# Kernel tuning notes

Measured on AMD Instinct MI355X. Metric: run time of the kernel, lower is better.

## Reference

```python
import jax, jax.numpy as jnp
import numpy as np

BIGNET_DIM = 1024
N_LAYERS = 18   # 6 blocks * 3 QLoRALinear
N_LN = 5
GROUPS = 64     # 1024 / group_size(16)
GS = 16
RANK = 32
BATCH = 16384
EPS = 1e-5


def dequant(qw, scale):
    # qw: [O, G, gs] int 0..15, scale: [O, G] per-group max-abs norm
    w = (qw.astype(jnp.float32) / 15.0 * 2.0 - 1.0) * scale[..., None]
    return w.reshape(qw.shape[0], -1)  # [O, I]


def qlora_linear(x, qw, scale, b, a_w, b_w):
    w = dequant(qw, scale)                      # [O, I]
    base = x @ w.T + b                          # [N, O]
    lora = (x @ a_w.T) @ b_w.T                  # [N, r] @ [r, O]
    return base + lora


def layernorm(h, g, b):
    mu = h.mean(-1, keepdims=True)
    var = jnp.mean((h - mu) ** 2, -1, keepdims=True)
    return (h - mu) * jax.lax.rsqrt(var + EPS) * g + b


def setup_inputs() -> dict:
    key = jax.random.key(0)
    ks = jax.random.split(key, 8)
    x = jax.random.normal(ks[0], (BATCH, BIGNET_DIM), jnp.float32)
    qw = jax.random.randint(ks[1], (N_LAYERS, BIGNET_DIM, GROUPS, GS), 0, 16, jnp.int32)
    scale = jax.random.uniform(ks[2], (N_LAYERS, BIGNET_DIM, GROUPS), jnp.float32) * 0.05
    bias = jax.random.normal(ks[3], (N_LAYERS, BIGNET_DIM), jnp.float32) * 0.02
    la = jax.random.normal(ks[4], (N_LAYERS, RANK, BIGNET_DIM), jnp.float32) * (2.0 / BIGNET_DIM) ** 0.5
    # note: torch zero-inits lora_b; use small random values so the LoRA path is testable
    lb = jax.random.normal(ks[5], (N_LAYERS, BIGNET_DIM, RANK), jnp.float32) * 0.01
    ln_w = jnp.ones((N_LN, BIGNET_DIM), jnp.float32)
    ln_b = jnp.zeros((N_LN, BIGNET_DIM), jnp.float32)
    return {"x": x, "scale": scale, "bias": bias, "la": la, "lb": lb,
            "ln_w": ln_w, "ln_b": ln_b, "qw": qw}


def reference(x, scale, bias, la, lb, ln_w, ln_b, qw):
    h = x
    li = 0
    for blk in range(6):
        r = h
        for j in range(3):
            h = qlora_linear(h, qw[li], scale[li], bias[li], la[li], lb[li])
            li += 1
            if j < 2:
                h = jax.nn.relu(h)
        h = h + r
        if blk < 5:
            h = layernorm(h, ln_w[blk], ln_b[blk])
    return h
```

## Files before the change

kernel.cpp:

```cpp
#include <hip/hip_runtime.h>

typedef unsigned short UST;
typedef __attribute__((ext_vector_type(8))) __bf16 bf16x8;
typedef __attribute__((ext_vector_type(4))) float f32x4;

__device__ __forceinline__ float bf2f(UST u) {
    union { unsigned int i; float f; } v; v.i = ((unsigned int)u) << 16; return v.f;
}
__device__ __forceinline__ UST f2bf(float f) {
    union { float f; unsigned int i; } v; v.f = f;
    return (UST)((v.i + 0x7fffu + ((v.i >> 16) & 1u)) >> 16);
}

__device__ __forceinline__ void gl2lds16(const UST* g, UST* l) {
    __builtin_amdgcn_global_load_lds(
        (const __attribute__((address_space(1))) unsigned int*)g,
        (__attribute__((address_space(3))) unsigned int*)l, 16, 0, 0);
}

__global__ __launch_bounds__(256) void prep_w(
    const int* __restrict__ qw, const float* __restrict__ scale,
    const float* __restrict__ la, const float* __restrict__ lb,
    UST* __restrict__ wp)
{
    int l = blockIdx.x, ot = blockIdx.y, it = blockIdx.z;
    __shared__ float la_s[32 * 128];
    __shared__ float lb_s[64 * 33];
    int t = threadIdx.x;
    int o0 = (t >> 4) * 4;
    int i0 = (t & 15) * 8;

    const int* qbase = qw + (size_t)l * 1048576 + (size_t)(ot * 64 + o0) * 1024
                       + it * 128 + i0;
    int4 qv[8];
    #pragma unroll
    for (int a = 0; a < 4; a++) {
        qv[2 * a]     = *(const int4*)(qbase + (size_t)a * 1024);
        qv[2 * a + 1] = *(const int4*)(qbase + (size_t)a * 1024 + 4);
    }
    const float* sL = scale + (size_t)l * 65536;
    float sc[4];
    #pragma unroll
    for (int a = 0; a < 4; a++)
        sc[a] = sL[(size_t)(ot * 64 + o0 + a) * 64 + ((it * 128 + i0) >> 4)];

    const float* laL = la + (size_t)l * 32768;
    const float* lbL = lb + (size_t)l * 32768 + (size_t)ot * 64 * 32;
    for (int e = t; e < 32 * 128; e += 256) {
        int r = e >> 7, i = e & 127;
        la_s[e] = laL[r * 1024 + it * 128 + i];
    }
    for (int e = t; e < 64 * 32; e += 256) {
        int o = e >> 5, r = e & 31;
        lb_s[o * 33 + r] = lbL[e];
    }
    __syncthreads();

    float acc[4][8];
    #pragma unroll
    for (int a = 0; a < 4; a++)
        #pragma unroll
        for (int c = 0; c < 8; c++) acc[a][c] = 0.f;
    for (int r = 0; r < 32; ++r) {
        float4 av0 = *(const float4*)&la_s[r * 128 + i0];
        float4 av1 = *(const float4*)&la_s[r * 128 + i0 + 4];
        float av[8] = {av0.x, av0.y, av0.z, av0.w, av1.x, av1.y, av1.z, av1.w};
        float bv[4];
        #pragma unroll
        for (int j = 0; j < 4; j++) bv[j] = lb_s[(o0 + j) * 33 + r];
        #pragma unroll
        for (int a = 0; a < 4; a++)
            #pragma unroll
            for (int c = 0; c < 8; c++) acc[a][c] += bv[a] * av[c];
    }

    UST* wL = wp + (size_t)l * 1048576;
    #pragma unroll
    for (int a = 0; a < 4; a++) {
        int go = ot * 64 + o0 + a;
        int gi = it * 128 + i0;
        float s = sc[a];
        int q[8];
        q[0] = qv[2 * a].x; q[1] = qv[2 * a].y; q[2] = qv[2 * a].z; q[3] = qv[2 * a].w;
        q[4] = qv[2 * a + 1].x; q[5] = qv[2 * a + 1].y;
        q[6] = qv[2 * a + 1].z; q[7] = qv[2 * a + 1].w;
        UST o8[8];
        #pragma unroll
        for (int c = 0; c < 8; c++) {
            float w = ((float)q[c] * (2.0f / 15.0f) - 1.0f) * s + acc[a][c];
            o8[c] = f2bf(w);
        }
        *(ushort4*)(wL + (size_t)go * 1024 + gi) = make_ushort4(o8[0], o8[1], o8[2], o8[3]);
        *(ushort4*)(wL + (size_t)go * 1024 + gi + 4) = make_ushort4(o8[4], o8[5], o8[6], o8[7]);
    }
}

__global__ __launch_bounds__(256) void f32_to_bf16(const float* __restrict__ x,
                                                   UST* __restrict__ o)
{
    size_t i = ((size_t)blockIdx.x * 256 + threadIdx.x) * 4;
    float4 v = *(const float4*)(x + i);
    *(ushort4*)(o + i) = make_ushort4(f2bf(v.x), f2bf(v.y), f2bf(v.z), f2bf(v.w));
}

#define BM 128
#define BN 128
#define BK 32

#define WB4 asm volatile("s_waitcnt vmcnt(4)\n\ts_barrier" ::: "memory")
#define WB0 asm volatile("s_waitcnt vmcnt(0)\n\ts_barrier" ::: "memory")
#define LGB asm volatile("s_waitcnt lgkmcnt(0)\n\ts_barrier" ::: "memory")

__global__ __launch_bounds__(256, 4) void gemm_ep(
    const UST* __restrict__ X, const UST* __restrict__ W,
    const float* __restrict__ bias,
    UST* __restrict__ outb, const UST* __restrict__ resid,
    float* __restrict__ outf, int mode)
{
    const int K = 1024;
    __shared__ UST smem[16384];
    int tid = threadIdx.x;
    int wave = tid >> 6, lane = tid & 63;
    int wm = wave >> 1, wn = wave & 1;

    int bid = blockIdx.x;
    int nbm8 = gridDim.x >> 6;
    int xcd = bid & 7, idx = bid >> 3;
    int bm = xcd + ((idx % nbm8) << 3);
    int bn = idx / nbm8;

    int la15 = lane & 15, qa = lane >> 4;

    int c0 = tid, c1 = tid + 256;
    int r0 = c0 >> 2, k0c = ((c0 & 3) ^ ((r0 >> 1) & 3)) * 8;
    int r1 = c1 >> 2, k1c = ((c1 & 3) ^ ((r1 >> 1) & 3)) * 8;
    const UST* gA0 = X + (size_t)(bm * BM + r0) * K + k0c;
    const UST* gA1 = X + (size_t)(bm * BM + r1) * K + k1c;
    const UST* gB0 = W + (size_t)(bn * BN + r0) * K + k0c;
    const UST* gB1 = W + (size_t)(bn * BN + r1) * K + k1c;

    int offA[4], offB[4];
    #pragma unroll
    for (int i = 0; i < 4; i++) {
        int ra = wm * 64 + i * 16 + la15;
        offA[i] = ra * 32 + ((qa ^ ((ra >> 1) & 3)) * 8);
        int rb = wn * 64 + i * 16 + la15;
        offB[i] = rb * 32 + ((qa ^ ((rb >> 1) & 3)) * 8);
    }

    f32x4 acc[4][4];
    #pragma unroll
    for (int i = 0; i < 4; i++)
        #pragma unroll
        for (int j = 0; j < 4; j++) acc[i][j] = (f32x4){0.f, 0.f, 0.f, 0.f};

    auto issue = [&](int kk, int buf) {
        UST* dA = smem + buf * 8192;
        UST* dB = dA + 4096;
        gl2lds16(gA0 + kk, dA + c0 * 8);
        gl2lds16(gA1 + kk, dA + c1 * 8);
        gl2lds16(gB0 + kk, dB + c0 * 8);
        gl2lds16(gB1 + kk, dB + c1 * 8);
    };
    auto compute = [&](int buf) {
        const UST* pA = smem + buf * 8192;
        const UST* pB = pA + 4096;
        bf16x8 af[4], bfr[4];
        #pragma unroll
        for (int mi = 0; mi < 4; mi++) af[mi] = *(const bf16x8*)&pA[offA[mi]];
        #pragma unroll
        for (int ni = 0; ni < 4; ni++) bfr[ni] = *(const bf16x8*)&pB[offB[ni]];
        #pragma unroll
        for (int mi = 0; mi < 4; mi++)
            #pragma unroll
            for (int ni = 0; ni < 4; ni++)
                acc[mi][ni] = __builtin_amdgcn_mfma_f32_16x16x32_bf16(
                    af[mi], bfr[ni], acc[mi][ni], 0, 0, 0);
    };

    issue(0, 0);
    #pragma unroll 2
    for (int it = 0; it < 31; ++it) {
        int cur = it & 1;
        issue((it + 1) * BK, cur ^ 1);
        WB4;
        compute(cur);
        LGB;
    }
    WB0;
    compute(1);
    LGB;

    float* cs = (float*)smem;
    int cc = tid & 15, rw = tid >> 4;
    int gcolb = bn * BN + cc * 8;
    float4 bv0 = *(const float4*)&bias[gcolb];
    float4 bv1 = *(const float4*)&bias[gcolb + 4];

    #pragma unroll
    for (int h = 0; h < 2; ++h) {
        if (wm == h) {
            #pragma unroll
            for (int mi = 0; mi < 4; mi++)
                #pragma unroll
                for (int ni = 0; ni < 4; ni++) {
                    int colx = (wn * 64 + ni * 16 + la15) ^ (qa << 4);
                    #pragma unroll
                    for (int r2 = 0; r2 < 4; r2++) {
                        int rl = mi * 16 + qa * 4 + r2;
                        cs[rl * 128 + colx] = acc[mi][ni][r2];
                    }
                }
        }
        LGB;
        #pragma unroll
        for (int g = 0; g < 4; ++g) {
            int rl = g * 16 + rw;
            int swz = ((rl >> 2) & 3) << 2;
            int gr0 = ((cc * 2) ^ swz) * 4;
            float4 v0 = *(const float4*)&cs[rl * 128 + gr0];
            float4 v1 = *(const float4*)&cs[rl * 128 + gr0 + 4];
            float o0 = v0.x + bv0.x, o1 = v0.y + bv0.y;
            float o2 = v0.z + bv0.z, o3 = v0.w + bv0.w;
            float o4 = v1.x + bv1.x, o5 = v1.y + bv1.y;
            float o6 = v1.z + bv1.z, o7 = v1.w + bv1.w;
            if (mode == 0) {
                o0 = fmaxf(o0, 0.f); o1 = fmaxf(o1, 0.f);
                o2 = fmaxf(o2, 0.f); o3 = fmaxf(o3, 0.f);
                o4 = fmaxf(o4, 0.f); o5 = fmaxf(o5, 0.f);
                o6 = fmaxf(o6, 0.f); o7 = fmaxf(o7, 0.f);
            }
            int grow = bm * BM + h * 64 + rl;
            size_t base = (size_t)grow * 1024 + gcolb;
            if (mode == 2) {
                ushort4 rv0 = *(const ushort4*)&resid[base];
                ushort4 rv1 = *(const ushort4*)&resid[base + 4];
                o0 += bf2f(rv0.x); o1 += bf2f(rv0.y);
                o2 += bf2f(rv0.z); o3 += bf2f(rv0.w);
                o4 += bf2f(rv1.x); o5 += bf2f(rv1.y);
                o6 += bf2f(rv1.z); o7 += bf2f(rv1.w);
                *(float4*)&outf[base] = make_float4(o0, o1, o2, o3);
                *(float4*)&outf[base + 4] = make_float4(o4, o5, o6, o7);
            } else {
                uint4 pk;
                pk.x = (unsigned)f2bf(o0) | ((unsigned)f2bf(o1) << 16);
                pk.y = (unsigned)f2bf(o2) | ((unsigned)f2bf(o3) << 16);
                pk.z = (unsigned)f2bf(o4) | ((unsigned)f2bf(o5) << 16);
                pk.w = (unsigned)f2bf(o6) | ((unsigned)f2bf(o7) << 16);
                *(uint4*)&outb[base] = pk;
            }
        }
        LGB;
    }
}

__global__ __launch_bounds__(256) void ln_res(
    const UST* __restrict__ h3, UST* __restrict__ r,
    const float* __restrict__ g, const float* __restrict__ b)
{
    int row = blockIdx.x;
    int t = threadIdx.x;
    int lane = t & 63, wave = t >> 6;
    const ushort4* hp = (const ushort4*)(h3 + (size_t)row * 1024);
    ushort4* rp = (ushort4*)(r + (size_t)row * 1024);
    ushort4 hv = hp[t], rv = rp[t];
    float u0 = bf2f(hv.x) + bf2f(rv.x);
    float u1 = bf2f(hv.y) + bf2f(rv.y);
    float u2 = bf2f(hv.z) + bf2f(rv.z);
    float u3 = bf2f(hv.w) + bf2f(rv.w);

    float s = u0 + u1 + u2 + u3;
    #pragma unroll
    for (int off = 32; off > 0; off >>= 1) s += __shfl_down(s, off, 64);
    __shared__ float red[8];
    if (lane == 0) red[wave] = s;
    __syncthreads();
    float mean = (red[0] + red[1] + red[2] + red[3]) * (1.0f / 1024.0f);

    float d0 = u0 - mean, d1 = u1 - mean, d2 = u2 - mean, d3 = u3 - mean;
    float vs = d0 * d0 + d1 * d1 + d2 * d2 + d3 * d3;
    #pragma unroll
    for (int off = 32; off > 0; off >>= 1) vs += __shfl_down(vs, off, 64);
    if (lane == 0) red[4 + wave] = vs;
    __syncthreads();
    float var = (red[4] + red[5] + red[6] + red[7]) * (1.0f / 1024.0f);
    float rstd = rsqrtf(var + 1e-5f);

    int i0 = t * 4;
    ushort4 o;
    o.x = f2bf(d0 * rstd * g[i0 + 0] + b[i0 + 0]);
    o.y = f2bf(d1 * rstd * g[i0 + 1] + b[i0 + 1]);
    o.z = f2bf(d2 * rstd * g[i0 + 2] + b[i0 + 2]);
    o.w = f2bf(d3 * rstd * g[i0 + 3] + b[i0 + 3]);
    rp[t] = o;
}

extern "C" void kernel_launch(void* const* d_in, const int* in_sizes, int n_in,
                              void* d_out, int out_size, void* d_ws, size_t ws_size,
                              hipStream_t stream) {
    const float* x     = (const float*)d_in[0];
    const float* scale = (const float*)d_in[1];
    const float* bias  = (const float*)d_in[2];
    const float* la    = (const float*)d_in[3];
    const float* lb    = (const float*)d_in[4];
    const float* ln_w  = (const float*)d_in[5];
    const float* ln_b  = (const float*)d_in[6];
    const int*   qw    = (const int*)d_in[7];

    const int M = in_sizes[0] / 1024;
    const size_t WPB = (size_t)18 * 1024 * 1024 * 2;
    const size_t ACT = (size_t)M * 1024 * 2;

    UST* wp = (UST*)d_ws;
    UST* A  = (UST*)((char*)d_ws + WPB);
    UST* Cb = (UST*)((char*)d_ws + WPB + ACT);
    UST* Bb = (UST*)d_out;

    prep_w<<<dim3(18, 16, 8), 256, 0, stream>>>(qw, scale, la, lb, wp);
    f32_to_bf16<<<(M * 1024) / (256 * 4), 256, 0, stream>>>(x, A);

    int nblk = (M / 128) * 8;
    int li = 0;
    for (int blk = 0; blk < 6; ++blk) {
        gemm_ep<<<nblk, 256, 0, stream>>>(
            A, wp + (size_t)li * 1024 * 1024, bias + li * 1024, Bb, nullptr, nullptr, 0);
        li++;
        gemm_ep<<<nblk, 256, 0, stream>>>(
            Bb, wp + (size_t)li * 1024 * 1024, bias + li * 1024, Cb, nullptr, nullptr, 0);
        li++;
        if (blk < 5) {
            gemm_ep<<<nblk, 256, 0, stream>>>(
                Cb, wp + (size_t)li * 1024 * 1024, bias + li * 1024, Bb, nullptr, nullptr, 1);
            li++;
            ln_res<<<M, 256, 0, stream>>>(Bb, A, ln_w + blk * 1024, ln_b + blk * 1024);
        } else {
            gemm_ep<<<nblk, 256, 0, stream>>>(
                Cb, wp + (size_t)li * 1024 * 1024, bias + li * 1024, nullptr, A,
                (float*)d_out, 2);
            li++;
        }
    }
}
```

Measured before the change: 1.097 ms.

## Enlarge GEMM tiles to 256x256 with 512 threads and MFMA-based weight prep

The main GEMM now uses a 256x256 output tile with 8 waves (512 threads), each wave computing 64x128. The goal is more reuse per LDS load and half as many global loads of A and W per output element. The weight-prep kernel now computes the LoRA product lb·la with bf16 MFMA instead of scalar FMAs and fuses dequantisation into an LDS-staged transposed store. The costs are higher register pressure (32 accumulators per wave), 64KB of LDS per block, and fewer blocks in the grid, which may lower occupancy. The LoRA product is also rounded to bf16 inputs before the matmul.

```diff
diff --git a/kernel.cpp b/kernel.cpp
--- a/kernel.cpp
+++ b/kernel.cpp
@@ -17,6 +17,10 @@
         (const __attribute__((address_space(1))) unsigned int*)g,
         (__attribute__((address_space(3))) unsigned int*)l, 16, 0, 0);
 }
+
+#define WB4 asm volatile("s_waitcnt vmcnt(4)\n\ts_barrier" ::: "memory")
+#define WB0 asm volatile("s_waitcnt vmcnt(0)\n\ts_barrier" ::: "memory")
+#define LGB asm volatile("s_waitcnt lgkmcnt(0)\n\ts_barrier" ::: "memory")
 
 __global__ __launch_bounds__(256) void prep_w(
     const int* __restrict__ qw, const float* __restrict__ scale,
@@ -24,179 +28,68 @@
     UST* __restrict__ wp)
 {
     int l = blockIdx.x, ot = blockIdx.y, it = blockIdx.z;
-    __shared__ float la_s[32 * 128];
-    __shared__ float lb_s[64 * 33];
+    __shared__ float cs[64 * 128];
+    __shared__ float sc_s[128 * 8];
     int t = threadIdx.x;
-    int o0 = (t >> 4) * 4;
-    int i0 = (t & 15) * 8;
-
-    const int* qbase = qw + (size_t)l * 1048576 + (size_t)(ot * 64 + o0) * 1024
-                       + it * 128 + i0;
-    int4 qv[8];
-    #pragma unroll
-    for (int a = 0; a < 4; a++) {
-        qv[2 * a]     = *(const int4*)(qbase + (size_t)a * 1024);
-        qv[2 * a + 1] = *(const int4*)(qbase + (size_t)a * 1024 + 4);
-    }
-    const float* sL = scale + (size_t)l * 65536;
-    float sc[4];
-    #pragma unroll
-    for (int a = 0; a < 4; a++)
-        sc[a] = sL[(size_t)(ot * 64 + o0 + a) * 64 + ((it * 128 + i0) >> 4)];
-
-    const float* laL = la + (size_t)l * 32768;
-    const float* lbL = lb + (size_t)l * 32768 + (size_t)ot * 64 * 32;
-    for (int e = t; e < 32 * 128; e += 256) {
-        int r = e >> 7, i = e & 127;
-        la_s[e] = laL[r * 1024 + it * 128 + i];
-    }
-    for (int e = t; e < 64 * 32; e += 256) {
-        int o = e >> 5, r = e & 31;
-        lb_s[o * 33 + r] = lbL[e];
-    }
+    int wave = t >> 6, lane = t & 63;
+    int wm = wave >> 1, wn = wave & 1;
+    int la15 = lane & 15, qa = lane >> 4;
+
+    {
+        int e = t * 4;
+        int o = e >> 3, g = e & 7;
+        const float* sb = scale + ((size_t)l * 1024 + ot * 128 + o) * 64 + it * 8 + g;
+        *(float4*)&sc_s[e] = *(const float4*)sb;
+    }
+
+    bf16x8 af[4];
+    const float* lbL = lb + ((size_t)l * 1024 + ot * 128 + wm * 64 + la15) * 32 + qa * 8;
+    #pragma unroll
+    for (int mi = 0; mi < 4; mi++) {
+        float4 u0 = *(const float4*)(lbL + mi * 16 * 32);
+        float4 u1 = *(const float4*)(lbL + mi * 16 * 32 + 4);
+        union { bf16x8 v; UST u[8]; } A;
+        A.u[0] = f2bf(u0.x); A.u[1] = f2bf(u0.y); A.u[2] = f2bf(u0.z); A.u[3] = f2bf(u0.w);
+        A.u[4] = f2bf(u1.x); A.u[5] = f2bf(u1.y); A.u[6] = f2bf(u1.z); A.u[7] = f2bf(u1.w);
+        af[mi] = A.v;
+    }
+
+    bf16x8 bfr[4];
+    const float* laL = la + ((size_t)l * 32 + qa * 8) * 1024 + it * 128 + wn * 64 + la15;
+    #pragma unroll
+    for (int ni = 0; ni < 4; ni++) {
+        union { bf16x8 v; UST u[8]; } B;
+        #pragma unroll
+        for (int j = 0; j < 8; j++) B.u[j] = f2bf(laL[(size_t)j * 1024 + ni * 16]);
+        bfr[ni] = B.v;
+    }
+
+    f32x4 acc[4][4];
+    #pragma unroll
+    for (int mi = 0; mi < 4; mi++)
+        #pragma unroll
+        for (int ni = 0; ni < 4; ni++) {
+            acc[mi][ni] = (f32x4){0.f, 0.f, 0.f, 0.f};
+            acc[mi][ni] = __builtin_amdgcn_mfma_f32_16x16x32_bf16(
+                af[mi], bfr[ni], acc[mi][ni], 0, 0, 0);
+        }
+
+    int qv[4][4][4];
+    const int* qL = qw + (size_t)l * 1048576;
+    int obase = ot * 128 + wm * 64, ibase = it * 128 + wn * 64;
+    #pragma unroll
+    for (int mi = 0; mi < 4; mi++)
+        #pragma unroll
+        for (int ni = 0; ni < 4; ni++)
+            #pragma unroll
+            for (int r2 = 0; r2 < 4; r2++)
+                qv[mi][ni][r2] = qL[(size_t)(obase + mi * 16 + qa * 4 + r2) * 1024
+                                    + ibase + ni * 16 + la15];
+
     __syncthreads();
 
-    float acc[4][8];
-    #pragma unroll
-    for (int a = 0; a < 4; a++)
-        #pragma unroll
-        for (int c = 0; c < 8; c++) acc[a][c] = 0.f;
-    for (int r = 0; r < 32; ++r) {
-        float4 av0 = *(const float4*)&la_s[r * 128 + i0];
-        float4 av1 = *(const float4*)&la_s[r * 128 + i0 + 4];
-        float av[8] = {av0.x, av0.y, av0.z, av0.w, av1.x, av1.y, av1.z, av1.w};
-        float bv[4];
-        #pragma unroll
-        for (int j = 0; j < 4; j++) bv[j] = lb_s[(o0 + j) * 33 + r];
-        #pragma unroll
-        for (int a = 0; a < 4; a++)
-            #pragma unroll
-            for (int c = 0; c < 8; c++) acc[a][c] += bv[a] * av[c];
-    }
-
+    int cc = t & 15, rw = t >> 4;
     UST* wL = wp + (size_t)l * 1048576;
-    #pragma unroll
-    for (int a = 0; a < 4; a++) {
-        int go = ot * 64 + o0 + a;
-        int gi = it * 128 + i0;
-        float s = sc[a];
-        int q[8];
-        q[0] = qv[2 * a].x; q[1] = qv[2 * a].y; q[2] = qv[2 * a].z; q[3] = qv[2 * a].w;
-        q[4] = qv[2 * a + 1].x; q[5] = qv[2 * a + 1].y;
-        q[6] = qv[2 * a + 1].z; q[7] = qv[2 * a + 1].w;
-        UST o8[8];
-        #pragma unroll
-        for (int c = 0; c < 8; c++) {
-            float w = ((float)q[c] * (2.0f / 15.0f) - 1.0f) * s + acc[a][c];
-            o8[c] = f2bf(w);
-        }
-        *(ushort4*)(wL + (size_t)go * 1024 + gi) = make_ushort4(o8[0], o8[1], o8[2], o8[3]);
-        *(ushort4*)(wL + (size_t)go * 1024 + gi + 4) = make_ushort4(o8[4], o8[5], o8[6], o8[7]);
-    }
-}
-
-__global__ __launch_bounds__(256) void f32_to_bf16(const float* __restrict__ x,
-                                                   UST* __restrict__ o)
-{
-    size_t i = ((size_t)blockIdx.x * 256 + threadIdx.x) * 4;
-    float4 v = *(const float4*)(x + i);
-    *(ushort4*)(o + i) = make_ushort4(f2bf(v.x), f2bf(v.y), f2bf(v.z), f2bf(v.w));
-}
-
-#define BM 128
-#define BN 128
-#define BK 32
-
-#define WB4 asm volatile("s_waitcnt vmcnt(4)\n\ts_barrier" ::: "memory")
-#define WB0 asm volatile("s_waitcnt vmcnt(0)\n\ts_barrier" ::: "memory")
-#define LGB asm volatile("s_waitcnt lgkmcnt(0)\n\ts_barrier" ::: "memory")
-
-__global__ __launch_bounds__(256, 4) void gemm_ep(
-    const UST* __restrict__ X, const UST* __restrict__ W,
-    const float* __restrict__ bias,
-    UST* __restrict__ outb, const UST* __restrict__ resid,
-    float* __restrict__ outf, int mode)
-{
-    const int K = 1024;
-    __shared__ UST smem[16384];
-    int tid = threadIdx.x;
-    int wave = tid >> 6, lane = tid & 63;
-    int wm = wave >> 1, wn = wave & 1;
-
-    int bid = blockIdx.x;
-    int nbm8 = gridDim.x >> 6;
-    int xcd = bid & 7, idx = bid >> 3;
-    int bm = xcd + ((idx % nbm8) << 3);
-    int bn = idx / nbm8;
-
-    int la15 = lane & 15, qa = lane >> 4;
-
-    int c0 = tid, c1 = tid + 256;
-    int r0 = c0 >> 2, k0c = ((c0 & 3) ^ ((r0 >> 1) & 3)) * 8;
-    int r1 = c1 >> 2, k1c = ((c1 & 3) ^ ((r1 >> 1) & 3)) * 8;
-    const UST* gA0 = X + (size_t)(bm * BM + r0) * K + k0c;
-    const UST* gA1 = X + (size_t)(bm * BM + r1) * K + k1c;
-    const UST* gB0 = W + (size_t)(bn * BN + r0) * K + k0c;
-    const UST* gB1 = W + (size_t)(bn * BN + r1) * K + k1c;
-
-    int offA[4], offB[4];
-    #pragma unroll
-    for (int i = 0; i < 4; i++) {
-        int ra = wm * 64 + i * 16 + la15;
-        offA[i] = ra * 32 + ((qa ^ ((ra >> 1) & 3)) * 8);
-        int rb = wn * 64 + i * 16 + la15;
-        offB[i] = rb * 32 + ((qa ^ ((rb >> 1) & 3)) * 8);
-    }
-
-    f32x4 acc[4][4];
-    #pragma unroll
-    for (int i = 0; i < 4; i++)
-        #pragma unroll
-        for (int j = 0; j < 4; j++) acc[i][j] = (f32x4){0.f, 0.f, 0.f, 0.f};
-
-    auto issue = [&](int kk, int buf) {
-        UST* dA = smem + buf * 8192;
-        UST* dB = dA + 4096;
-        gl2lds16(gA0 + kk, dA + c0 * 8);
-        gl2lds16(gA1 + kk, dA + c1 * 8);
-        gl2lds16(gB0 + kk, dB + c0 * 8);
-        gl2lds16(gB1 + kk, dB + c1 * 8);
-    };
-    auto compute = [&](int buf) {
-        const UST* pA = smem + buf * 8192;
-        const UST* pB = pA + 4096;
-        bf16x8 af[4], bfr[4];
-        #pragma unroll
-        for (int mi = 0; mi < 4; mi++) af[mi] = *(const bf16x8*)&pA[offA[mi]];
-        #pragma unroll
-        for (int ni = 0; ni < 4; ni++) bfr[ni] = *(const bf16x8*)&pB[offB[ni]];
-        #pragma unroll
-        for (int mi = 0; mi < 4; mi++)
-            #pragma unroll
-            for (int ni = 0; ni < 4; ni++)
-                acc[mi][ni] = __builtin_amdgcn_mfma_f32_16x16x32_bf16(
-                    af[mi], bfr[ni], acc[mi][ni], 0, 0, 0);
-    };
-
-    issue(0, 0);
-    #pragma unroll 2
-    for (int it = 0; it < 31; ++it) {
-        int cur = it & 1;
-        issue((it + 1) * BK, cur ^ 1);
-        WB4;
-        compute(cur);
-        LGB;
-    }
-    WB0;
-    compute(1);
-    LGB;
-
-    float* cs = (float*)smem;
-    int cc = tid & 15, rw = tid >> 4;
-    int gcolb = bn * BN + cc * 8;
-    float4 bv0 = *(const float4*)&bias[gcolb];
-    float4 bv1 = *(const float4*)&bias[gcolb + 4];
-
     #pragma unroll
     for (int h = 0; h < 2; ++h) {
         if (wm == h) {
@@ -208,7 +101,10 @@
                     #pragma unroll
                     for (int r2 = 0; r2 < 4; r2++) {
                         int rl = mi * 16 + qa * 4 + r2;
-                        cs[rl * 128 + colx] = acc[mi][ni][r2];
+                        float s = sc_s[(h * 64 + rl) * 8 + wn * 4 + ni];
+                        float w = ((float)qv[mi][ni][r2] * (2.0f / 15.0f) - 1.0f) * s
+                                  + acc[mi][ni][r2];
+                        cs[rl * 128 + colx] = w;
                     }
                 }
         }
@@ -220,6 +116,137 @@
             int gr0 = ((cc * 2) ^ swz) * 4;
             float4 v0 = *(const float4*)&cs[rl * 128 + gr0];
             float4 v1 = *(const float4*)&cs[rl * 128 + gr0 + 4];
+            uint4 pk;
+            pk.x = (unsigned)f2bf(v0.x) | ((unsigned)f2bf(v0.y) << 16);
+            pk.y = (unsigned)f2bf(v0.z) | ((unsigned)f2bf(v0.w) << 16);
+            pk.z = (unsigned)f2bf(v1.x) | ((unsigned)f2bf(v1.y) << 16);
+            pk.w = (unsigned)f2bf(v1.z) | ((unsigned)f2bf(v1.w) << 16);
+            *(uint4*)&wL[(size_t)(ot * 128 + h * 64 + rl) * 1024 + it * 128 + cc * 8] = pk;
+        }
+        LGB;
+    }
+}
+
+__global__ __launch_bounds__(256) void f32_to_bf16(const float* __restrict__ x,
+                                                   UST* __restrict__ o)
+{
+    size_t i = ((size_t)blockIdx.x * 256 + threadIdx.x) * 4;
+    float4 v = *(const float4*)(x + i);
+    *(ushort4*)(o + i) = make_ushort4(f2bf(v.x), f2bf(v.y), f2bf(v.z), f2bf(v.w));
+}
+
+#define BK 32
+
+__global__ __launch_bounds__(512, 2) void gemm_ep(
+    const UST* __restrict__ X, const UST* __restrict__ W,
+    const float* __restrict__ bias,
+    UST* __restrict__ outb, const UST* __restrict__ resid,
+    float* __restrict__ outf, int mode)
+{
+    const int K = 1024;
+    __shared__ UST smem[32768];
+    int tid = threadIdx.x;
+    int wave = tid >> 6, lane = tid & 63;
+    int wm = wave >> 1, wn = wave & 1;
+    int la15 = lane & 15, qa = lane >> 4;
+
+    int bid = blockIdx.x;
+    int xcd = bid & 7, idx = bid >> 3;
+    int bm = xcd * 8 + (idx & 7);
+    int bn = idx >> 3;
+
+    int c0 = tid, c1 = tid + 512;
+    int r0 = c0 >> 2, k0c = ((c0 & 3) ^ ((r0 >> 1) & 3)) * 8;
+    int r1 = c1 >> 2, k1c = ((c1 & 3) ^ ((r1 >> 1) & 3)) * 8;
+    const UST* gA0 = X + (size_t)(bm * 256 + r0) * K + k0c;
+    const UST* gA1 = X + (size_t)(bm * 256 + r1) * K + k1c;
+    const UST* gB0 = W + (size_t)(bn * 256 + r0) * K + k0c;
+    const UST* gB1 = W + (size_t)(bn * 256 + r1) * K + k1c;
+
+    int offA[4], offB[8];
+    #pragma unroll
+    for (int i = 0; i < 4; i++) {
+        int ra = wm * 64 + i * 16 + la15;
+        offA[i] = ra * 32 + ((qa ^ ((ra >> 1) & 3)) * 8);
+    }
+    #pragma unroll
+    for (int i = 0; i < 8; i++) {
+        int rb = wn * 128 + i * 16 + la15;
+        offB[i] = rb * 32 + ((qa ^ ((rb >> 1) & 3)) * 8);
+    }
+
+    f32x4 acc[4][8];
+    #pragma unroll
+    for (int i = 0; i < 4; i++)
+        #pragma unroll
+        for (int j = 0; j < 8; j++) acc[i][j] = (f32x4){0.f, 0.f, 0.f, 0.f};
+
+    auto issue = [&](int kk, int buf) {
+        UST* dA = smem + buf * 16384;
+        UST* dB = dA + 8192;
+        gl2lds16(gA0 + kk, dA + c0 * 8);
+        gl2lds16(gA1 + kk, dA + c1 * 8);
+        gl2lds16(gB0 + kk, dB + c0 * 8);
+        gl2lds16(gB1 + kk, dB + c1 * 8);
+    };
+    auto compute = [&](int buf) {
+        const UST* pA = smem + buf * 16384;
+        const UST* pB = pA + 8192;
+        bf16x8 af[4], bfr[8];
+        #pragma unroll
+        for (int mi = 0; mi < 4; mi++) af[mi] = *(const bf16x8*)&pA[offA[mi]];
+        #pragma unroll
+        for (int ni = 0; ni < 8; ni++) bfr[ni] = *(const bf16x8*)&pB[offB[ni]];
+        #pragma unroll
+        for (int mi = 0; mi < 4; mi++)
+            #pragma unroll
+            for (int ni = 0; ni < 8; ni++)
+                acc[mi][ni] = __builtin_amdgcn_mfma_f32_16x16x32_bf16(
+                    af[mi], bfr[ni], acc[mi][ni], 0, 0, 0);
+    };
+
+    issue(0, 0);
+    #pragma unroll 2
+    for (int it = 0; it < 31; ++it) {
+        int cur = it & 1;
+        issue((it + 1) * BK, cur ^ 1);
+        WB4;
+        compute(cur);
+        LGB;
+    }
+    WB0;
+    compute(1);
+    LGB;
+
+    float* cs = (float*)smem;
+    int cc = tid & 31, rw = tid >> 5;
+    int gcolb = bn * 256 + cc * 8;
+    float4 bv0 = *(const float4*)&bias[gcolb];
+    float4 bv1 = *(const float4*)&bias[gcolb + 4];
+
+    #pragma unroll
+    for (int h = 0; h < 4; ++h) {
+        if (wm == h) {
+            #pragma unroll
+            for (int mi = 0; mi < 4; mi++)
+                #pragma unroll
+                for (int ni = 0; ni < 8; ni++) {
+                    int colx = (wn * 128 + ni * 16 + la15) ^ (qa << 4);
+                    #pragma unroll
+                    for (int r2 = 0; r2 < 4; r2++) {
+                        int rl = mi * 16 + qa * 4 + r2;
+                        cs[rl * 256 + colx] = acc[mi][ni][r2];
+                    }
+                }
+        }
+        LGB;
+        #pragma unroll
+        for (int g = 0; g < 4; ++g) {
+            int rl = g * 16 + rw;
+            int swz = ((rl >> 2) & 3) << 2;
+            int gr0 = ((cc * 2) ^ swz) * 4;
+            float4 v0 = *(const float4*)&cs[rl * 256 + gr0];
+            float4 v1 = *(const float4*)&cs[rl * 256 + gr0 + 4];
             float o0 = v0.x + bv0.x, o1 = v0.y + bv0.y;
             float o2 = v0.z + bv0.z, o3 = v0.w + bv0.w;
             float o4 = v1.x + bv1.x, o5 = v1.y + bv1.y;
@@ -230,7 +257,7 @@
                 o4 = fmaxf(o4, 0.f); o5 = fmaxf(o5, 0.f);
                 o6 = fmaxf(o6, 0.f); o7 = fmaxf(o7, 0.f);
             }
-            int grow = bm * BM + h * 64 + rl;
+            int grow = bm * 256 + h * 64 + rl;
             size_t base = (size_t)grow * 1024 + gcolb;
             if (mode == 2) {
                 ushort4 rv0 = *(const ushort4*)&resid[base];
@@ -316,25 +343,25 @@
     UST* Cb = (UST*)((char*)d_ws + WPB + ACT);
     UST* Bb = (UST*)d_out;
 
-    prep_w<<<dim3(18, 16, 8), 256, 0, stream>>>(qw, scale, la, lb, wp);
+    prep_w<<<dim3(18, 8, 8), 256, 0, stream>>>(qw, scale, la, lb, wp);
     f32_to_bf16<<<(M * 1024) / (256 * 4), 256, 0, stream>>>(x, A);
 
-    int nblk = (M / 128) * 8;
+    int nblk = (M / 256) * 4;
     int li = 0;
     for (int blk = 0; blk < 6; ++blk) {
-        gemm_ep<<<nblk, 256, 0, stream>>>(
+        gemm_ep<<<nblk, 512, 0, stream>>>(
             A, wp + (size_t)li * 1024 * 1024, bias + li * 1024, Bb, nullptr, nullptr, 0);
         li++;
-        gemm_ep<<<nblk, 256, 0, stream>>>(
+        gemm_ep<<<nblk, 512, 0, stream>>>(
             Bb, wp + (size_t)li * 1024 * 1024, bias + li * 1024, Cb, nullptr, nullptr, 0);
         li++;
         if (blk < 5) {
-            gemm_ep<<<nblk, 256, 0, stream>>>(
+            gemm_ep<<<nblk, 512, 0, stream>>>(
                 Cb, wp + (size_t)li * 1024 * 1024, bias + li * 1024, Bb, nullptr, nullptr, 1);
             li++;
             ln_res<<<M, 256, 0, stream>>>(Bb, A, ln_w + blk * 1024, ln_b + blk * 1024);
         } else {
-            gemm_ep<<<nblk, 256, 0, stream>>>(
+            gemm_ep<<<nblk, 512, 0, stream>>>(
                 Cb, wp + (size_t)li * 1024 * 1024, bias + li * 1024, nullptr, A,
                 (float*)d_out, 2);
             li++;
```

New measurement: 953.4 us. 13.1% less time.
